# Kernel optimization log

Measured on AMD Instinct MI355X. Metric: run time of the kernel, lower is better.

Reference implementation:

```python
import jax, jax.numpy as jnp
import numpy as np

N_NODES = 100000
N_EDGES = 1600000
N_FEAT = 128
HIDDEN = 128
N_CLASSES = 64


def setup_inputs() -> dict:
    key = jax.random.key(0)
    ks = jax.random.split(key, 6)
    x = jax.random.normal(ks[0], (N_NODES, N_FEAT), dtype=jnp.float32)
    edge_index = jax.random.randint(ks[1], (2, N_EDGES), 0, N_NODES, dtype=jnp.int64)
    # Glorot-ish scaled weights
    W1_l = jax.random.normal(ks[2], (N_FEAT, HIDDEN), dtype=jnp.float32) / np.sqrt(N_FEAT)
    W1_r = jax.random.normal(ks[3], (N_FEAT, HIDDEN), dtype=jnp.float32) / np.sqrt(N_FEAT)
    W2_l = jax.random.normal(ks[4], (HIDDEN, N_CLASSES), dtype=jnp.float32) / np.sqrt(HIDDEN)
    W2_r = jax.random.normal(ks[5], (HIDDEN, N_CLASSES), dtype=jnp.float32) / np.sqrt(HIDDEN)
    b1 = jnp.zeros((HIDDEN,), dtype=jnp.float32)
    b2 = jnp.zeros((N_CLASSES,), dtype=jnp.float32)
    return {"x": x, "edge_index": edge_index, "W1_l": W1_l, "b1": b1,
            "W1_r": W1_r, "W2_l": W2_l, "b2": b2, "W2_r": W2_r}


def _sage_conv(h, src, dst, n_nodes, inv_deg, W_l, W_r, b):
    # mean aggregation of source-node features into destination nodes
    agg = jax.ops.segment_sum(h[src], dst, num_segments=n_nodes)  # [N, d]
    agg = agg * inv_deg[:, None]
    return agg @ W_l + h @ W_r + b


def reference(x, edge_index, W1_l, b1, W1_r, W2_l, b2, W2_r):
    src, dst = edge_index[0], edge_index[1]
    n = x.shape[0]
    deg = jax.ops.segment_sum(jnp.ones_like(dst, dtype=x.dtype), dst, num_segments=n)
    inv_deg = 1.0 / jnp.maximum(deg, 1.0)
    h = jax.nn.relu(_sage_conv(x, src, dst, n, inv_deg, W1_l, W1_r, b1))
    # dropout is identity in eval mode
    out = _sage_conv(h, src, dst, n, inv_deg, W2_l, W2_r, b2)
    return out
```

## Files before the change

kernel.cpp:

```cpp
#include <hip/hip_runtime.h>

#define N_NODES   100000
#define N_EDGES   1600000
#define BSHIFT    9
#define NB        196
#define BSTRIDE   9216

typedef __attribute__((ext_vector_type(8))) short short8;
typedef __attribute__((ext_vector_type(4))) float f32x4;
typedef __attribute__((ext_vector_type(2))) float f32x2;

__device__ __forceinline__ unsigned short f2bf(float f) {
    unsigned u = __float_as_uint(f);
    u += 0x7FFF + ((u >> 16) & 1);
    return (unsigned short)(u >> 16);
}

__device__ __forceinline__ int load_src(const int* e, int is64, int i) {
    return is64 ? e[2 * i] : e[i];
}
__device__ __forceinline__ int load_dst(const int* e, int is64, int i) {
    return is64 ? e[2 * (N_EDGES + i)] : e[N_EDGES + i];
}

__device__ __forceinline__ int block_detect_is64(const int* e, int* s_nz) {
    if (threadIdx.x == 0) *s_nz = 0;
    __syncthreads();
    int v = 0;
    for (int i = threadIdx.x; i < 1024; i += 256) v |= e[2 * i + 1];
    if (v) atomicOr(s_nz, 1);
    __syncthreads();
    return (*s_nz == 0) ? 1 : 0;
}

__global__ __launch_bounds__(256) void phaseA_kernel(
        const int* __restrict__ e, const float* __restrict__ x,
        const float* __restrict__ W1_l, const float* __restrict__ W1_r,
        const float* __restrict__ W2_l, const float* __restrict__ W2_r,
        int* __restrict__ bktcur, int* __restrict__ pairs,
        short* __restrict__ xb, unsigned int* __restrict__ xq,
        short* __restrict__ W1t, short* __restrict__ W2lt, short* __restrict__ W2rt) {
    __shared__ int2 s_pairs[4096];
    __shared__ int s_cnt[256], s_off[256], s_base[256], s_cur[256];
    __shared__ int s_nz;
    const int blk = blockIdx.x;
    if (blk < 391) {
        const int tid = threadIdx.x;
        s_cnt[tid] = 0;
        int is64 = block_detect_is64(e, &s_nz);
        __syncthreads();
        int i0 = blk * 4096;
        int n = min(4096, N_EDGES - i0);
        int ls[16], ld[16];
        #pragma unroll
        for (int t = 0; t < 16; t++) {
            int k = t * 256 + tid;
            if (k < n) {
                ls[t] = load_src(e, is64, i0 + k);
                ld[t] = load_dst(e, is64, i0 + k);
                atomicAdd(&s_cnt[ld[t] >> BSHIFT], 1);
            }
        }
        __syncthreads();
        int lv = s_cnt[tid];
        s_off[tid] = lv;
        __syncthreads();
        for (int off = 1; off < 256; off <<= 1) {
            int t = (tid >= off) ? s_off[tid - off] : 0;
            __syncthreads();
            s_off[tid] += t;
            __syncthreads();
        }
        int excl = s_off[tid] - lv;
        int gb = 0;
        if (tid < NB && lv > 0) gb = atomicAdd(&bktcur[tid], lv);
        s_off[tid] = excl;
        s_base[tid] = tid * BSTRIDE + gb;
        s_cur[tid] = excl;
        __syncthreads();
        #pragma unroll
        for (int t = 0; t < 16; t++) {
            int k = t * 256 + tid;
            if (k < n) {
                int pos = atomicAdd(&s_cur[ld[t] >> BSHIFT], 1);
                s_pairs[pos] = (int2){ls[t], ld[t]};
            }
        }
        __syncthreads();
        for (int j = tid; j < n; j += 256) {
            int2 pr = s_pairs[j];
            int b = pr.y >> BSHIFT;
            pairs[s_base[b] + (j - s_off[b])] = pr.x | ((pr.y & 511) << 17);
        }
    } else if (blk < 12891) {
        int t = (blk - 391) * 256 + threadIdx.x;
        int i = t * 4;
        float4 v = *(const float4*)&x[i];
        short4 o;
        o.x = (short)f2bf(v.x); o.y = (short)f2bf(v.y);
        o.z = (short)f2bf(v.z); o.w = (short)f2bf(v.w);
        *(short4*)&xb[i] = o;
        int w = __builtin_amdgcn_cvt_pk_fp8_f32(v.x, v.y, 0, false);
        w = __builtin_amdgcn_cvt_pk_fp8_f32(v.z, v.w, w, true);
        xq[t] = (unsigned int)w;
    } else {
        int i = (blk - 12891) * 256 + threadIdx.x;
        if (i < 32768) {
            int n = i >> 8, k = i & 255;
            float v = (k < 128) ? W1_l[k * 128 + n] : W1_r[(k - 128) * 128 + n];
            W1t[i] = (short)f2bf(v);
        } else if (i < 40960) {
            int j = i - 32768, n = j >> 7, k = j & 127;
            W2lt[j] = (short)f2bf(W2_l[k * 64 + n]);
        } else {
            int j = i - 40960, n = j >> 7, k = j & 127;
            W2rt[j] = (short)f2bf(W2_r[k * 64 + n]);
        }
    }
}

__global__ __launch_bounds__(512) void fused_fill_kernel(
        const int* __restrict__ bktcur, const int* __restrict__ pairs,
        int* __restrict__ deg_i, int* __restrict__ cursor,
        float* __restrict__ inv_deg, int* __restrict__ col) {
    __shared__ int ldeg[512];
    __shared__ int ssum[512];
    const int tid = threadIdx.x;
    const int b = blockIdx.x;
    const int nbase = b << BSHIFT;
    ldeg[tid] = 0;
    __syncthreads();
    const int cnt = bktcur[b];
    const int p0 = b * BSTRIDE;
    for (int j = tid; j < cnt; j += 512)
        atomicAdd(&ldeg[pairs[p0 + j] >> 17], 1);
    __syncthreads();
    int d = ldeg[tid];
    ssum[tid] = d;
    __syncthreads();
    for (int off = 1; off < 512; off <<= 1) {
        int t = (tid >= off) ? ssum[tid - off] : 0;
        __syncthreads();
        ssum[tid] += t;
        __syncthreads();
    }
    int s = p0 + ssum[tid] - d;
    int node = nbase + tid;
    if (node < N_NODES) {
        deg_i[node] = d;
        cursor[node] = s;
        inv_deg[node] = 1.0f / fmaxf((float)d, 1.0f);
    }
    ldeg[tid] = s;
    __syncthreads();
    for (int j = tid; j < cnt; j += 512) {
        int pk = pairs[p0 + j];
        int pos = atomicAdd(&ldeg[pk >> 17], 1);
        col[pos] = pk & 0x1FFFF;
    }
}

__device__ __forceinline__ void acc_fp8x8(float* acc, uint2 w) {
    f32x2 f;
    f = __builtin_amdgcn_cvt_pk_f32_fp8((int)w.x, false); acc[0] += f[0]; acc[1] += f[1];
    f = __builtin_amdgcn_cvt_pk_f32_fp8((int)w.x, true);  acc[2] += f[0]; acc[3] += f[1];
    f = __builtin_amdgcn_cvt_pk_f32_fp8((int)w.y, false); acc[4] += f[0]; acc[5] += f[1];
    f = __builtin_amdgcn_cvt_pk_f32_fp8((int)w.y, true);  acc[6] += f[0]; acc[7] += f[1];
}

__global__ __launch_bounds__(256) void agg128_kernel(
        const int* __restrict__ cursor, const int* __restrict__ deg_i,
        const int* __restrict__ col, const unsigned int* __restrict__ xq,
        const float* __restrict__ inv_deg, short* __restrict__ agg) {
    int node = blockIdx.x * 16 + (threadIdx.x >> 4);
    int lane = threadIdx.x & 15;
    int cnt = deg_i[node];
    int start = cursor[node];
    float acc[8] = {0.f};
    int k = 0;
    for (; k + 4 <= cnt; k += 4) {
        int s0 = col[start + k + 0];
        int s1 = col[start + k + 1];
        int s2 = col[start + k + 2];
        int s3 = col[start + k + 3];
        uint2 w0 = *(const uint2*)(xq + (size_t)s0 * 32 + lane * 2);
        uint2 w1 = *(const uint2*)(xq + (size_t)s1 * 32 + lane * 2);
        uint2 w2 = *(const uint2*)(xq + (size_t)s2 * 32 + lane * 2);
        uint2 w3 = *(const uint2*)(xq + (size_t)s3 * 32 + lane * 2);
        acc_fp8x8(acc, w0); acc_fp8x8(acc, w1);
        acc_fp8x8(acc, w2); acc_fp8x8(acc, w3);
    }
    for (; k < cnt; k++) {
        int s0 = col[start + k];
        uint2 w = *(const uint2*)(xq + (size_t)s0 * 32 + lane * 2);
        acc_fp8x8(acc, w);
    }
    float sc = inv_deg[node];
    short8 o;
    #pragma unroll
    for (int j = 0; j < 8; j++) o[j] = (short)f2bf(acc[j] * sc);
    *(short8*)(agg + (size_t)node * 128 + lane * 8) = o;
}

__global__ __launch_bounds__(256) void agg64_kernel(
        const int* __restrict__ cursor, const int* __restrict__ deg_i,
        const int* __restrict__ col, const unsigned int* __restrict__ pq,
        const float* __restrict__ inv_deg, float* __restrict__ out) {
    int node = blockIdx.x * 32 + (threadIdx.x >> 3);
    int lane = threadIdx.x & 7;
    int cnt = deg_i[node];
    int start = cursor[node];
    float acc[8] = {0.f};
    int k = 0;
    for (; k + 4 <= cnt; k += 4) {
        int s0 = col[start + k + 0];
        int s1 = col[start + k + 1];
        int s2 = col[start + k + 2];
        int s3 = col[start + k + 3];
        uint2 w0 = *(const uint2*)(pq + (size_t)s0 * 16 + lane * 2);
        uint2 w1 = *(const uint2*)(pq + (size_t)s1 * 16 + lane * 2);
        uint2 w2 = *(const uint2*)(pq + (size_t)s2 * 16 + lane * 2);
        uint2 w3 = *(const uint2*)(pq + (size_t)s3 * 16 + lane * 2);
        acc_fp8x8(acc, w0); acc_fp8x8(acc, w1);
        acc_fp8x8(acc, w2); acc_fp8x8(acc, w3);
    }
    for (; k < cnt; k++) {
        int s0 = col[start + k];
        uint2 w = *(const uint2*)(pq + (size_t)s0 * 16 + lane * 2);
        acc_fp8x8(acc, w);
    }
    float sc = inv_deg[node];
    float* dst = out + (size_t)node * 64 + lane * 8;
    float4 o0 = *(float4*)dst;
    float4 o1 = *(float4*)(dst + 4);
    o0.x += acc[0] * sc; o0.y += acc[1] * sc; o0.z += acc[2] * sc; o0.w += acc[3] * sc;
    o1.x += acc[4] * sc; o1.y += acc[5] * sc; o1.z += acc[6] * sc; o1.w += acc[7] * sc;
    *(float4*)dst = o0;
    *(float4*)(dst + 4) = o1;
}

__global__ __launch_bounds__(256, 2) void gemm12_mfma(
        const short* __restrict__ agg1, const short* __restrict__ xb,
        const short* __restrict__ W1t, const float* __restrict__ b1,
        const short* __restrict__ W2lt, const short* __restrict__ W2rt,
        const float* __restrict__ b2,
        unsigned char* __restrict__ p8, float* __restrict__ out) {
    __shared__ __align__(16) char hs[2][8192];
    const int wave = threadIdx.x >> 6, lane = threadIdx.x & 63;
    const int m = lane & 15, q = lane >> 4;

    short8 breg[2][8];
    #pragma unroll
    for (int t = 0; t < 2; t++)
        #pragma unroll
        for (int c = 0; c < 8; c++)
            breg[t][c] = *(const short8*)(W1t + (size_t)(wave * 32 + t * 16 + m) * 256 + c * 32 + q * 8);
    float bias1[2];
    bias1[0] = b1[wave * 32 + m];
    bias1[1] = b1[wave * 32 + 16 + m];

    const int pw = wave & 1;
    const short* Wp = (wave < 2) ? W2lt : W2rt;
    short8 w2[2][4];
    #pragma unroll
    for (int t = 0; t < 2; t++)
        #pragma unroll
        for (int c = 0; c < 4; c++)
            w2[t][c] = *(const short8*)(Wp + (size_t)(pw * 32 + t * 16 + m) * 128 + c * 32 + q * 8);
    float bias2[2];
    bias2[0] = b2[pw * 32 + m];
    bias2[1] = b2[pw * 32 + 16 + m];

    int P = blockIdx.x;
    short8 a[2][8];
    #pragma unroll
    for (int tt = 0; tt < 2; tt++) {
        const short* arow = agg1 + (size_t)((2 * P + tt) * 16 + m) * 128;
        const short* xrow = xb   + (size_t)((2 * P + tt) * 16 + m) * 128;
        #pragma unroll
        for (int c = 0; c < 4; c++) {
            a[tt][c]     = *(const short8*)(arow + c * 32 + q * 8);
            a[tt][c + 4] = *(const short8*)(xrow + c * 32 + q * 8);
        }
    }
    const int wb = wave * 64 + m * 2;
    const int rsw = (m & 7) << 4;
    int buf = 0;
    while (true) {
        f32x4 acc[2][2];
        #pragma unroll
        for (int tt = 0; tt < 2; tt++)
            #pragma unroll
            for (int t = 0; t < 2; t++) acc[tt][t] = (f32x4){0.f, 0.f, 0.f, 0.f};
        #pragma unroll
        for (int c = 0; c < 8; c++)
            #pragma unroll
            for (int tt = 0; tt < 2; tt++)
                #pragma unroll
                for (int t = 0; t < 2; t++)
                    acc[tt][t] = __builtin_amdgcn_mfma_f32_16x16x32_bf16(a[tt][c], breg[t][c], acc[tt][t], 0, 0, 0);
        int Pn = P + 512;
        if (Pn < 3125) {
            #pragma unroll
            for (int tt = 0; tt < 2; tt++) {
                const short* arow = agg1 + (size_t)((2 * Pn + tt) * 16 + m) * 128;
                const short* xrow = xb   + (size_t)((2 * Pn + tt) * 16 + m) * 128;
                #pragma unroll
                for (int c = 0; c < 4; c++) {
                    a[tt][c]     = *(const short8*)(arow + c * 32 + q * 8);
                    a[tt][c + 4] = *(const short8*)(xrow + c * 32 + q * 8);
                }
            }
        }
        char* hb0 = hs[buf];
        #pragma unroll
        for (int tt = 0; tt < 2; tt++)
            #pragma unroll
            for (int t = 0; t < 2; t++)
                #pragma unroll
                for (int r = 0; r < 4; r++) {
                    int row = tt * 16 + q * 4 + r;
                    int byteoff = row * 256 + ((wb + t * 32) ^ ((row & 7) << 4));
                    float v = fmaxf(acc[tt][t][r] + bias1[t], 0.f);
                    *(short*)(hb0 + byteoff) = (short)f2bf(v);
                }
        __syncthreads();
        f32x4 acc2[2][2];
        #pragma unroll
        for (int tt = 0; tt < 2; tt++) {
            short8 a2[4];
            int rowbyte = (tt * 16 + m) * 256;
            #pragma unroll
            for (int c = 0; c < 4; c++)
                a2[c] = *(const short8*)(hb0 + rowbyte + ((q * 16 + c * 64) ^ rsw));
            #pragma unroll
            for (int t = 0; t < 2; t++) acc2[tt][t] = (f32x4){0.f, 0.f, 0.f, 0.f};
            #pragma unroll
            for (int c = 0; c < 4; c++)
                #pragma unroll
                for (int t = 0; t < 2; t++)
                    acc2[tt][t] = __builtin_amdgcn_mfma_f32_16x16x32_bf16(a2[c], w2[t][c], acc2[tt][t], 0, 0, 0);
        }
        if (wave < 2) {
            #pragma unroll
            for (int tt = 0; tt < 2; tt++)
                #pragma unroll
                for (int t = 0; t < 2; t++) {
                    int colc = pw * 32 + t * 16 + m;
                    #pragma unroll
                    for (int r = 0; r < 4; r++) {
                        int rr = (2 * P + tt) * 16 + q * 4 + r;
                        float pv = acc2[tt][t][r];
                        int w8 = __builtin_amdgcn_cvt_pk_fp8_f32(pv, pv, 0, false);
                        p8[(size_t)rr * 64 + colc] = (unsigned char)(w8 & 0xFF);
                    }
                }
        } else {
            #pragma unroll
            for (int tt = 0; tt < 2; tt++)
                #pragma unroll
                for (int t = 0; t < 2; t++) {
                    int colc = pw * 32 + t * 16 + m;
                    #pragma unroll
                    for (int r = 0; r < 4; r++) {
                        int rr = (2 * P + tt) * 16 + q * 4 + r;
                        out[(size_t)rr * 64 + colc] = acc2[tt][t][r] + bias2[t];
                    }
                }
        }
        if (Pn >= 3125) break;
        P = Pn;
        buf ^= 1;
    }
}

extern "C" void kernel_launch(void* const* d_in, const int* in_sizes, int n_in,
                              void* d_out, int out_size, void* d_ws, size_t ws_size,
                              hipStream_t stream) {
    const float* x    = (const float*)d_in[0];
    const int*   edge = (const int*)d_in[1];
    const float* W1_l = (const float*)d_in[2];
    const float* b1   = (const float*)d_in[3];
    const float* W1_r = (const float*)d_in[4];
    const float* W2_l = (const float*)d_in[5];
    const float* b2   = (const float*)d_in[6];
    const float* W2_r = (const float*)d_in[7];
    float* out = (float*)d_out;

    int* iw = (int*)d_ws;
    int* deg_i  = iw;
    int* cursor = iw + 100000;
    int* bktcur = iw + 200000;
    float* inv_deg = (float*)(iw + 200256);
    int* col    = iw + 300352;
    short* xb   = (short*)(iw + 2106688);
    short* hb   = xb + 12800000;
    short* ag1  = hb + 12800000;
    short* W1t  = ag1 + 12800000;
    short* W2lt = W1t + 32768;
    short* W2rt = W2lt + 8192;
    unsigned int* xq = (unsigned int*)hb;
    int* pairs = (int*)ag1;
    unsigned char* p8 = (unsigned char*)hb;
    unsigned int*  pq = (unsigned int*)hb;

    hipMemsetAsync(bktcur, 0, 256 * sizeof(int), stream);

    phaseA_kernel<<<13083, 256, 0, stream>>>(edge, x, W1_l, W1_r, W2_l, W2_r,
                                             bktcur, pairs, xb, xq, W1t, W2lt, W2rt);
    fused_fill_kernel<<<NB, 512, 0, stream>>>(bktcur, pairs, deg_i, cursor, inv_deg, col);

    agg128_kernel<<<6250, 256, 0, stream>>>(cursor, deg_i, col, xq, inv_deg, ag1);
    gemm12_mfma<<<512, 256, 0, stream>>>(ag1, xb, W1t, b1, W2lt, W2rt, b2, p8, out);
    agg64_kernel<<<3125, 256, 0, stream>>>(cursor, deg_i, col, pq, inv_deg, out);
}
```

Measured before the change: 239.6 us.

## Fuse layer-1 neighbor aggregation into the MFMA GEMM kernel via LDS

```diff
diff --git a/kernel.cpp b/kernel.cpp
--- a/kernel.cpp
+++ b/kernel.cpp
@@ -167,39 +167,9 @@
     f = __builtin_amdgcn_cvt_pk_f32_fp8((int)w.y, false); acc[4] += f[0]; acc[5] += f[1];
     f = __builtin_amdgcn_cvt_pk_f32_fp8((int)w.y, true);  acc[6] += f[0]; acc[7] += f[1];
 }
-
-__global__ __launch_bounds__(256) void agg128_kernel(
-        const int* __restrict__ cursor, const int* __restrict__ deg_i,
-        const int* __restrict__ col, const unsigned int* __restrict__ xq,
-        const float* __restrict__ inv_deg, short* __restrict__ agg) {
-    int node = blockIdx.x * 16 + (threadIdx.x >> 4);
-    int lane = threadIdx.x & 15;
-    int cnt = deg_i[node];
-    int start = cursor[node];
-    float acc[8] = {0.f};
-    int k = 0;
-    for (; k + 4 <= cnt; k += 4) {
-        int s0 = col[start + k + 0];
-        int s1 = col[start + k + 1];
-        int s2 = col[start + k + 2];
-        int s3 = col[start + k + 3];
-        uint2 w0 = *(const uint2*)(xq + (size_t)s0 * 32 + lane * 2);
-        uint2 w1 = *(const uint2*)(xq + (size_t)s1 * 32 + lane * 2);
-        uint2 w2 = *(const uint2*)(xq + (size_t)s2 * 32 + lane * 2);
-        uint2 w3 = *(const uint2*)(xq + (size_t)s3 * 32 + lane * 2);
-        acc_fp8x8(acc, w0); acc_fp8x8(acc, w1);
-        acc_fp8x8(acc, w2); acc_fp8x8(acc, w3);
-    }
-    for (; k < cnt; k++) {
-        int s0 = col[start + k];
-        uint2 w = *(const uint2*)(xq + (size_t)s0 * 32 + lane * 2);
-        acc_fp8x8(acc, w);
-    }
-    float sc = inv_deg[node];
-    short8 o;
-    #pragma unroll
-    for (int j = 0; j < 8; j++) o[j] = (short)f2bf(acc[j] * sc);
-    *(short8*)(agg + (size_t)node * 128 + lane * 8) = o;
+__device__ __forceinline__ void acc_fp8x16(float* acc, uint4 w) {
+    acc_fp8x8(acc,     (uint2){w.x, w.y});
+    acc_fp8x8(acc + 8, (uint2){w.z, w.w});
 }
 
 __global__ __launch_bounds__(256) void agg64_kernel(
@@ -239,14 +209,19 @@
     *(float4*)(dst + 4) = o1;
 }
 
-__global__ __launch_bounds__(256, 2) void gemm12_mfma(
-        const short* __restrict__ agg1, const short* __restrict__ xb,
+__global__ __launch_bounds__(256, 2) void gemm12_fused(
+        const int* __restrict__ cursor, const int* __restrict__ deg_i,
+        const int* __restrict__ col, const unsigned int* __restrict__ xq,
+        const float* __restrict__ inv_deg,
+        const short* __restrict__ xb,
         const short* __restrict__ W1t, const float* __restrict__ b1,
         const short* __restrict__ W2lt, const short* __restrict__ W2rt,
         const float* __restrict__ b2,
         unsigned char* __restrict__ p8, float* __restrict__ out) {
-    __shared__ __align__(16) char hs[2][8192];
-    const int wave = threadIdx.x >> 6, lane = threadIdx.x & 63;
+    __shared__ __align__(16) char aLDS[8192];
+    __shared__ __align__(16) char hsb[8192];
+    const int tid = threadIdx.x;
+    const int wave = tid >> 6, lane = tid & 63;
     const int m = lane & 15, q = lane >> 4;
 
     short8 breg[2][8];
@@ -271,48 +246,81 @@
     bias2[0] = b2[pw * 32 + m];
     bias2[1] = b2[pw * 32 + 16 + m];
 
-    int P = blockIdx.x;
-    short8 a[2][8];
-    #pragma unroll
-    for (int tt = 0; tt < 2; tt++) {
-        const short* arow = agg1 + (size_t)((2 * P + tt) * 16 + m) * 128;
-        const short* xrow = xb   + (size_t)((2 * P + tt) * 16 + m) * 128;
-        #pragma unroll
-        for (int c = 0; c < 4; c++) {
-            a[tt][c]     = *(const short8*)(arow + c * 32 + q * 8);
-            a[tt][c + 4] = *(const short8*)(xrow + c * 32 + q * 8);
-        }
-    }
+    const int rsw = (m & 7) << 4;
     const int wb = wave * 64 + m * 2;
-    const int rsw = (m & 7) << 4;
-    int buf = 0;
-    while (true) {
-        f32x4 acc[2][2];
+
+    for (int P = blockIdx.x; P < 3125; P += 512) {
+        short8 ax[2][4];
+        #pragma unroll
+        for (int tt = 0; tt < 2; tt++) {
+            const short* xrow = xb + (size_t)((2 * P + tt) * 16 + m) * 128;
+            #pragma unroll
+            for (int c = 0; c < 4; c++)
+                ax[tt][c] = *(const short8*)(xrow + c * 32 + q * 8);
+        }
+        {
+            const int nl = tid >> 3;
+            const int l8 = tid & 7;
+            const int node = P * 32 + nl;
+            const int cnt = deg_i[node];
+            const int start = cursor[node];
+            float acc[16];
+            #pragma unroll
+            for (int j = 0; j < 16; j++) acc[j] = 0.f;
+            int k = 0;
+            for (; k + 4 <= cnt; k += 4) {
+                int s0 = col[start + k + 0];
+                int s1 = col[start + k + 1];
+                int s2 = col[start + k + 2];
+                int s3 = col[start + k + 3];
+                uint4 w0 = *(const uint4*)(xq + (size_t)s0 * 32 + l8 * 4);
+                uint4 w1 = *(const uint4*)(xq + (size_t)s1 * 32 + l8 * 4);
+                uint4 w2v = *(const uint4*)(xq + (size_t)s2 * 32 + l8 * 4);
+                uint4 w3 = *(const uint4*)(xq + (size_t)s3 * 32 + l8 * 4);
+                acc_fp8x16(acc, w0); acc_fp8x16(acc, w1);
+                acc_fp8x16(acc, w2v); acc_fp8x16(acc, w3);
+            }
+            for (; k < cnt; k++) {
+                uint4 w = *(const uint4*)(xq + (size_t)col[start + k] * 32 + l8 * 4);
+                acc_fp8x16(acc, w);
+            }
+            float sc = inv_deg[node];
+            short8 o0, o1;
+            #pragma unroll
+            for (int j = 0; j < 8; j++) {
+                o0[j] = (short)f2bf(acc[j] * sc);
+                o1[j] = (short)f2bf(acc[8 + j] * sc);
+            }
+            int r7 = nl & 7;
+            *(short8*)(aLDS + nl * 256 + ((l8 * 2)     ^ r7) * 16) = o0;
+            *(short8*)(aLDS + nl * 256 + ((l8 * 2 + 1) ^ r7) * 16) = o1;
+        }
+        __syncthreads();
+        f32x4 acc1[2][2];
         #pragma unroll
         for (int tt = 0; tt < 2; tt++)
             #pragma unroll
-            for (int t = 0; t < 2; t++) acc[tt][t] = (f32x4){0.f, 0.f, 0.f, 0.f};
-        #pragma unroll
-        for (int c = 0; c < 8; c++)
+            for (int t = 0; t < 2; t++) acc1[tt][t] = (f32x4){0.f, 0.f, 0.f, 0.f};
+        #pragma unroll
+        for (int tt = 0; tt < 2; tt++) {
+            short8 ag[4];
+            int rowbyte = (tt * 16 + m) * 256;
+            #pragma unroll
+            for (int c = 0; c < 4; c++)
+                ag[c] = *(const short8*)(aLDS + rowbyte + ((q * 16 + c * 64) ^ rsw));
+            #pragma unroll
+            for (int c = 0; c < 4; c++)
+                #pragma unroll
+                for (int t = 0; t < 2; t++)
+                    acc1[tt][t] = __builtin_amdgcn_mfma_f32_16x16x32_bf16(ag[c], breg[t][c], acc1[tt][t], 0, 0, 0);
+        }
+        #pragma unroll
+        for (int c = 0; c < 4; c++)
             #pragma unroll
             for (int tt = 0; tt < 2; tt++)
                 #pragma unroll
                 for (int t = 0; t < 2; t++)
-                    acc[tt][t] = __builtin_amdgcn_mfma_f32_16x16x32_bf16(a[tt][c], breg[t][c], acc[tt][t], 0, 0, 0);
-        int Pn = P + 512;
-        if (Pn < 3125) {
-            #pragma unroll
-            for (int tt = 0; tt < 2; tt++) {
-                const short* arow = agg1 + (size_t)((2 * Pn + tt) * 16 + m) * 128;
-                const short* xrow = xb   + (size_t)((2 * Pn + tt) * 16 + m) * 128;
-                #pragma unroll
-                for (int c = 0; c < 4; c++) {
-                    a[tt][c]     = *(const short8*)(arow + c * 32 + q * 8);
-                    a[tt][c + 4] = *(const short8*)(xrow + c * 32 + q * 8);
-                }
-            }
-        }
-        char* hb0 = hs[buf];
+                    acc1[tt][t] = __builtin_amdgcn_mfma_f32_16x16x32_bf16(ax[tt][c], breg[t][c + 4], acc1[tt][t], 0, 0, 0);
         #pragma unroll
         for (int tt = 0; tt < 2; tt++)
             #pragma unroll
@@ -321,8 +329,8 @@
                 for (int r = 0; r < 4; r++) {
                     int row = tt * 16 + q * 4 + r;
                     int byteoff = row * 256 + ((wb + t * 32) ^ ((row & 7) << 4));
-                    float v = fmaxf(acc[tt][t][r] + bias1[t], 0.f);
-                    *(short*)(hb0 + byteoff) = (short)f2bf(v);
+                    float v = fmaxf(acc1[tt][t][r] + bias1[t], 0.f);
+                    *(short*)(hsb + byteoff) = (short)f2bf(v);
                 }
         __syncthreads();
         f32x4 acc2[2][2];
@@ -332,7 +340,7 @@
             int rowbyte = (tt * 16 + m) * 256;
             #pragma unroll
             for (int c = 0; c < 4; c++)
-                a2[c] = *(const short8*)(hb0 + rowbyte + ((q * 16 + c * 64) ^ rsw));
+                a2[c] = *(const short8*)(hsb + rowbyte + ((q * 16 + c * 64) ^ rsw));
             #pragma unroll
             for (int t = 0; t < 2; t++) acc2[tt][t] = (f32x4){0.f, 0.f, 0.f, 0.f};
             #pragma unroll
@@ -368,9 +376,7 @@
                     }
                 }
         }
-        if (Pn >= 3125) break;
-        P = Pn;
-        buf ^= 1;
+        __syncthreads();
     }
 }
 
@@ -395,14 +401,14 @@
     int* col    = iw + 300352;
     short* xb   = (short*)(iw + 2106688);
     short* hb   = xb + 12800000;
-    short* ag1  = hb + 12800000;
-    short* W1t  = ag1 + 12800000;
+    short* rg3  = hb + 12800000;
+    short* W1t  = rg3 + 12800000;
     short* W2lt = W1t + 32768;
     short* W2rt = W2lt + 8192;
     unsigned int* xq = (unsigned int*)hb;
-    int* pairs = (int*)ag1;
-    unsigned char* p8 = (unsigned char*)hb;
-    unsigned int*  pq = (unsigned int*)hb;
+    int* pairs = (int*)rg3;
+    unsigned char* p8 = (unsigned char*)rg3;
+    unsigned int*  pq = (unsigned int*)rg3;
 
     hipMemsetAsync(bktcur, 0, 256 * sizeof(int), stream);
 
@@ -410,7 +416,7 @@
                                              bktcur, pairs, xb, xq, W1t, W2lt, W2rt);
     fused_fill_kernel<<<NB, 512, 0, stream>>>(bktcur, pairs, deg_i, cursor, inv_deg, col);
 
-    agg128_kernel<<<6250, 256, 0, stream>>>(cursor, deg_i, col, xq, inv_deg, ag1);
-    gemm12_mfma<<<512, 256, 0, stream>>>(ag1, xb, W1t, b1, W2lt, W2rt, b2, p8, out);
+    gemm12_fused<<<512, 256, 0, stream>>>(cursor, deg_i, col, xq, inv_deg,
+                                          xb, W1t, b1, W2lt, W2rt, b2, p8, out);
     agg64_kernel<<<3125, 256, 0, stream>>>(cursor, deg_i, col, pq, inv_deg, out);
 }
```

Result: no change. 242.3 us (+1.1%).

## Unroll gather loops to 8 and make GEMM kernel one tile per block

Applied to the files above, without the earlier changes.

```diff
diff --git a/kernel.cpp b/kernel.cpp
--- a/kernel.cpp
+++ b/kernel.cpp
@@ -178,21 +178,19 @@
     int start = cursor[node];
     float acc[8] = {0.f};
     int k = 0;
-    for (; k + 4 <= cnt; k += 4) {
-        int s0 = col[start + k + 0];
-        int s1 = col[start + k + 1];
-        int s2 = col[start + k + 2];
-        int s3 = col[start + k + 3];
-        uint2 w0 = *(const uint2*)(xq + (size_t)s0 * 32 + lane * 2);
-        uint2 w1 = *(const uint2*)(xq + (size_t)s1 * 32 + lane * 2);
-        uint2 w2 = *(const uint2*)(xq + (size_t)s2 * 32 + lane * 2);
-        uint2 w3 = *(const uint2*)(xq + (size_t)s3 * 32 + lane * 2);
-        acc_fp8x8(acc, w0); acc_fp8x8(acc, w1);
-        acc_fp8x8(acc, w2); acc_fp8x8(acc, w3);
+    for (; k + 8 <= cnt; k += 8) {
+        int s[8];
+        #pragma unroll
+        for (int j = 0; j < 8; j++) s[j] = col[start + k + j];
+        uint2 w[8];
+        #pragma unroll
+        for (int j = 0; j < 8; j++)
+            w[j] = *(const uint2*)(xq + (size_t)s[j] * 32 + lane * 2);
+        #pragma unroll
+        for (int j = 0; j < 8; j++) acc_fp8x8(acc, w[j]);
     }
     for (; k < cnt; k++) {
-        int s0 = col[start + k];
-        uint2 w = *(const uint2*)(xq + (size_t)s0 * 32 + lane * 2);
+        uint2 w = *(const uint2*)(xq + (size_t)col[start + k] * 32 + lane * 2);
         acc_fp8x8(acc, w);
     }
     float sc = inv_deg[node];
@@ -210,167 +208,137 @@
     int lane = threadIdx.x & 7;
     int cnt = deg_i[node];
     int start = cursor[node];
+    float sc = inv_deg[node];
+    float* dst = out + (size_t)node * 64 + lane * 8;
+    float4 r0 = *(float4*)dst;
+    float4 r1 = *(float4*)(dst + 4);
     float acc[8] = {0.f};
     int k = 0;
-    for (; k + 4 <= cnt; k += 4) {
-        int s0 = col[start + k + 0];
-        int s1 = col[start + k + 1];
-        int s2 = col[start + k + 2];
-        int s3 = col[start + k + 3];
-        uint2 w0 = *(const uint2*)(pq + (size_t)s0 * 16 + lane * 2);
-        uint2 w1 = *(const uint2*)(pq + (size_t)s1 * 16 + lane * 2);
-        uint2 w2 = *(const uint2*)(pq + (size_t)s2 * 16 + lane * 2);
-        uint2 w3 = *(const uint2*)(pq + (size_t)s3 * 16 + lane * 2);
-        acc_fp8x8(acc, w0); acc_fp8x8(acc, w1);
-        acc_fp8x8(acc, w2); acc_fp8x8(acc, w3);
+    for (; k + 8 <= cnt; k += 8) {
+        int s[8];
+        #pragma unroll
+        for (int j = 0; j < 8; j++) s[j] = col[start + k + j];
+        uint2 w[8];
+        #pragma unroll
+        for (int j = 0; j < 8; j++)
+            w[j] = *(const uint2*)(pq + (size_t)s[j] * 16 + lane * 2);
+        #pragma unroll
+        for (int j = 0; j < 8; j++) acc_fp8x8(acc, w[j]);
     }
     for (; k < cnt; k++) {
-        int s0 = col[start + k];
-        uint2 w = *(const uint2*)(pq + (size_t)s0 * 16 + lane * 2);
+        uint2 w = *(const uint2*)(pq + (size_t)col[start + k] * 16 + lane * 2);
         acc_fp8x8(acc, w);
     }
-    float sc = inv_deg[node];
-    float* dst = out + (size_t)node * 64 + lane * 8;
-    float4 o0 = *(float4*)dst;
-    float4 o1 = *(float4*)(dst + 4);
-    o0.x += acc[0] * sc; o0.y += acc[1] * sc; o0.z += acc[2] * sc; o0.w += acc[3] * sc;
-    o1.x += acc[4] * sc; o1.y += acc[5] * sc; o1.z += acc[6] * sc; o1.w += acc[7] * sc;
-    *(float4*)dst = o0;
-    *(float4*)(dst + 4) = o1;
-}
-
-__global__ __launch_bounds__(256, 2) void gemm12_mfma(
+    r0.x += acc[0] * sc; r0.y += acc[1] * sc; r0.z += acc[2] * sc; r0.w += acc[3] * sc;
+    r1.x += acc[4] * sc; r1.y += acc[5] * sc; r1.z += acc[6] * sc; r1.w += acc[7] * sc;
+    *(float4*)dst = r0;
+    *(float4*)(dst + 4) = r1;
+}
+
+__global__ __launch_bounds__(256, 4) void gemm12_mfma(
         const short* __restrict__ agg1, const short* __restrict__ xb,
         const short* __restrict__ W1t, const float* __restrict__ b1,
         const short* __restrict__ W2lt, const short* __restrict__ W2rt,
         const float* __restrict__ b2,
         unsigned char* __restrict__ p8, float* __restrict__ out) {
-    __shared__ __align__(16) char hs[2][8192];
+    __shared__ __align__(16) char hsb[8192];
     const int wave = threadIdx.x >> 6, lane = threadIdx.x & 63;
     const int m = lane & 15, q = lane >> 4;
-
-    short8 breg[2][8];
-    #pragma unroll
-    for (int t = 0; t < 2; t++)
-        #pragma unroll
-        for (int c = 0; c < 8; c++)
-            breg[t][c] = *(const short8*)(W1t + (size_t)(wave * 32 + t * 16 + m) * 256 + c * 32 + q * 8);
+    const int P = blockIdx.x;
+
+    short8 a[2][8];
+    #pragma unroll
+    for (int tt = 0; tt < 2; tt++) {
+        const short* arow = agg1 + (size_t)((2 * P + tt) * 16 + m) * 128;
+        const short* xrow = xb   + (size_t)((2 * P + tt) * 16 + m) * 128;
+        #pragma unroll
+        for (int c = 0; c < 4; c++) {
+            a[tt][c]     = *(const short8*)(arow + c * 32 + q * 8);
+            a[tt][c + 4] = *(const short8*)(xrow + c * 32 + q * 8);
+        }
+    }
     float bias1[2];
     bias1[0] = b1[wave * 32 + m];
     bias1[1] = b1[wave * 32 + 16 + m];
 
+    f32x4 acc1[2][2];
+    #pragma unroll
+    for (int tt = 0; tt < 2; tt++)
+        #pragma unroll
+        for (int t = 0; t < 2; t++) acc1[tt][t] = (f32x4){0.f, 0.f, 0.f, 0.f};
+    #pragma unroll
+    for (int c = 0; c < 8; c++) {
+        short8 br0 = *(const short8*)(W1t + (size_t)(wave * 32 + m) * 256 + c * 32 + q * 8);
+        short8 br1 = *(const short8*)(W1t + (size_t)(wave * 32 + 16 + m) * 256 + c * 32 + q * 8);
+        #pragma unroll
+        for (int tt = 0; tt < 2; tt++) {
+            acc1[tt][0] = __builtin_amdgcn_mfma_f32_16x16x32_bf16(a[tt][c], br0, acc1[tt][0], 0, 0, 0);
+            acc1[tt][1] = __builtin_amdgcn_mfma_f32_16x16x32_bf16(a[tt][c], br1, acc1[tt][1], 0, 0, 0);
+        }
+    }
+    const int wb = wave * 64 + m * 2;
+    #pragma unroll
+    for (int tt = 0; tt < 2; tt++)
+        #pragma unroll
+        for (int t = 0; t < 2; t++)
+            #pragma unroll
+            for (int r = 0; r < 4; r++) {
+                int row = tt * 16 + q * 4 + r;
+                int byteoff = row * 256 + ((wb + t * 32) ^ ((row & 7) << 4));
+                float v = fmaxf(acc1[tt][t][r] + bias1[t], 0.f);
+                *(short*)(hsb + byteoff) = (short)f2bf(v);
+            }
+    __syncthreads();
     const int pw = wave & 1;
     const short* Wp = (wave < 2) ? W2lt : W2rt;
-    short8 w2[2][4];
-    #pragma unroll
-    for (int t = 0; t < 2; t++)
-        #pragma unroll
-        for (int c = 0; c < 4; c++)
-            w2[t][c] = *(const short8*)(Wp + (size_t)(pw * 32 + t * 16 + m) * 128 + c * 32 + q * 8);
     float bias2[2];
     bias2[0] = b2[pw * 32 + m];
     bias2[1] = b2[pw * 32 + 16 + m];
-
-    int P = blockIdx.x;
-    short8 a[2][8];
+    const int rsw = (m & 7) << 4;
+    f32x4 acc2[2][2];
     #pragma unroll
     for (int tt = 0; tt < 2; tt++) {
-        const short* arow = agg1 + (size_t)((2 * P + tt) * 16 + m) * 128;
-        const short* xrow = xb   + (size_t)((2 * P + tt) * 16 + m) * 128;
+        short8 a2[4];
+        int rowbyte = (tt * 16 + m) * 256;
+        #pragma unroll
+        for (int c = 0; c < 4; c++)
+            a2[c] = *(const short8*)(hsb + rowbyte + ((q * 16 + c * 64) ^ rsw));
+        #pragma unroll
+        for (int t = 0; t < 2; t++) acc2[tt][t] = (f32x4){0.f, 0.f, 0.f, 0.f};
         #pragma unroll
         for (int c = 0; c < 4; c++) {
-            a[tt][c]     = *(const short8*)(arow + c * 32 + q * 8);
-            a[tt][c + 4] = *(const short8*)(xrow + c * 32 + q * 8);
-        }
-    }
-    const int wb = wave * 64 + m * 2;
-    const int rsw = (m & 7) << 4;
-    int buf = 0;
-    while (true) {
-        f32x4 acc[2][2];
+            short8 w20 = *(const short8*)(Wp + (size_t)(pw * 32 + m) * 128 + c * 32 + q * 8);
+            short8 w21 = *(const short8*)(Wp + (size_t)(pw * 32 + 16 + m) * 128 + c * 32 + q * 8);
+            acc2[tt][0] = __builtin_amdgcn_mfma_f32_16x16x32_bf16(a2[c], w20, acc2[tt][0], 0, 0, 0);
+            acc2[tt][1] = __builtin_amdgcn_mfma_f32_16x16x32_bf16(a2[c], w21, acc2[tt][1], 0, 0, 0);
+        }
+    }
+    if (wave < 2) {
         #pragma unroll
         for (int tt = 0; tt < 2; tt++)
             #pragma unroll
-            for (int t = 0; t < 2; t++) acc[tt][t] = (f32x4){0.f, 0.f, 0.f, 0.f};
-        #pragma unroll
-        for (int c = 0; c < 8; c++)
-            #pragma unroll
-            for (int tt = 0; tt < 2; tt++)
+            for (int t = 0; t < 2; t++) {
+                int colc = pw * 32 + t * 16 + m;
                 #pragma unroll
-                for (int t = 0; t < 2; t++)
-                    acc[tt][t] = __builtin_amdgcn_mfma_f32_16x16x32_bf16(a[tt][c], breg[t][c], acc[tt][t], 0, 0, 0);
-        int Pn = P + 512;
-        if (Pn < 3125) {
-            #pragma unroll
-            for (int tt = 0; tt < 2; tt++) {
-                const short* arow = agg1 + (size_t)((2 * Pn + tt) * 16 + m) * 128;
-                const short* xrow = xb   + (size_t)((2 * Pn + tt) * 16 + m) * 128;
-                #pragma unroll
-                for (int c = 0; c < 4; c++) {
-                    a[tt][c]     = *(const short8*)(arow + c * 32 + q * 8);
-                    a[tt][c + 4] = *(const short8*)(xrow + c * 32 + q * 8);
+                for (int r = 0; r < 4; r++) {
+                    int rr = (2 * P + tt) * 16 + q * 4 + r;
+                    float pv = acc2[tt][t][r];
+                    int w8 = __builtin_amdgcn_cvt_pk_fp8_f32(pv, pv, 0, false);
+                    p8[(size_t)rr * 64 + colc] = (unsigned char)(w8 & 0xFF);
                 }
             }
-        }
-        char* hb0 = hs[buf];
+    } else {
         #pragma unroll
         for (int tt = 0; tt < 2; tt++)
             #pragma unroll
-            for (int t = 0; t < 2; t++)
+            for (int t = 0; t < 2; t++) {
+                int colc = pw * 32 + t * 16 + m;
                 #pragma unroll
                 for (int r = 0; r < 4; r++) {
-                    int row = tt * 16 + q * 4 + r;
-                    int byteoff = row * 256 + ((wb + t * 32) ^ ((row & 7) << 4));
-                    float v = fmaxf(acc[tt][t][r] + bias1[t], 0.f);
-                    *(short*)(hb0 + byteoff) = (short)f2bf(v);
+                    int rr = (2 * P + tt) * 16 + q * 4 + r;
+                    out[(size_t)rr * 64 + colc] = acc2[tt][t][r] + bias2[t];
                 }
-        __syncthreads();
-        f32x4 acc2[2][2];
-        #pragma unroll
-        for (int tt = 0; tt < 2; tt++) {
-            short8 a2[4];
-            int rowbyte = (tt * 16 + m) * 256;
-            #pragma unroll
-            for (int c = 0; c < 4; c++)
-                a2[c] = *(const short8*)(hb0 + rowbyte + ((q * 16 + c * 64) ^ rsw));
-            #pragma unroll
-            for (int t = 0; t < 2; t++) acc2[tt][t] = (f32x4){0.f, 0.f, 0.f, 0.f};
-            #pragma unroll
-            for (int c = 0; c < 4; c++)
-                #pragma unroll
-                for (int t = 0; t < 2; t++)
-                    acc2[tt][t] = __builtin_amdgcn_mfma_f32_16x16x32_bf16(a2[c], w2[t][c], acc2[tt][t], 0, 0, 0);
-        }
-        if (wave < 2) {
-            #pragma unroll
-            for (int tt = 0; tt < 2; tt++)
-                #pragma unroll
-                for (int t = 0; t < 2; t++) {
-                    int colc = pw * 32 + t * 16 + m;
-                    #pragma unroll
-                    for (int r = 0; r < 4; r++) {
-                        int rr = (2 * P + tt) * 16 + q * 4 + r;
-                        float pv = acc2[tt][t][r];
-                        int w8 = __builtin_amdgcn_cvt_pk_fp8_f32(pv, pv, 0, false);
-                        p8[(size_t)rr * 64 + colc] = (unsigned char)(w8 & 0xFF);
-                    }
-                }
-        } else {
-            #pragma unroll
-            for (int tt = 0; tt < 2; tt++)
-                #pragma unroll
-                for (int t = 0; t < 2; t++) {
-                    int colc = pw * 32 + t * 16 + m;
-                    #pragma unroll
-                    for (int r = 0; r < 4; r++) {
-                        int rr = (2 * P + tt) * 16 + q * 4 + r;
-                        out[(size_t)rr * 64 + colc] = acc2[tt][t][r] + bias2[t];
-                    }
-                }
-        }
-        if (Pn >= 3125) break;
-        P = Pn;
-        buf ^= 1;
+            }
     }
 }
 
@@ -411,6 +379,6 @@
     fused_fill_kernel<<<NB, 512, 0, stream>>>(bktcur, pairs, deg_i, cursor, inv_deg, col);
 
     agg128_kernel<<<6250, 256, 0, stream>>>(cursor, deg_i, col, xq, inv_deg, ag1);
-    gemm12_mfma<<<512, 256, 0, stream>>>(ag1, xb, W1t, b1, W2lt, W2rt, b2, p8, out);
+    gemm12_mfma<<<3125, 256, 0, stream>>>(ag1, xb, W1t, b1, W2lt, W2rt, b2, p8, out);
     agg64_kernel<<<3125, 256, 0, stream>>>(cursor, deg_i, col, pq, inv_deg, out);
 }
```

Result: slower. 268.9 us (+12.2%).
